# Optimization experiments

Hardware: AMD Instinct MI355X
Metric: run time of the kernel (lower is better)

## Reference

```python
import jax, jax.numpy as jnp
import numpy as np

LEAK = 0.95
THRESHOLD = 1.0
RESCALE = 2.0


def _xavier_uniform(key, shape, gain=2.0):
    fan_out, fan_in = shape
    bound = gain * np.sqrt(6.0 / (fan_in + fan_out))
    return jax.random.uniform(key, shape, jnp.float32, -bound, bound)


def setup_inputs() -> dict:
    key = jax.random.key(0)
    k_inp, k_w1, k_w2 = jax.random.split(key, 3)
    inp = jax.random.normal(k_inp, (8192, 784), jnp.float32)
    w1 = _xavier_uniform(k_w1, (800, 784))   # fc1.weight
    w2 = _xavier_uniform(k_w2, (10, 800))    # fc2.weight
    return {"inp": inp, "w1": w1, "w2": w2, "num_steps": 25}


@jax.custom_vjp
def spike_fn(x):
    return (x > 0).astype(x.dtype)

def _spike_fwd(x):
    return spike_fn(x), x

def _spike_bwd(x, g):
    # grad = g * 0.3 * relu(1 - |x|)  (surrogate BP)
    return (g * 0.3 * jnp.maximum(1.0 - jnp.abs(x), 0.0),)

spike_fn.defvjp(_spike_fwd, _spike_bwd)


def poisson_gen(key, inp):
    r = jax.random.uniform(key, inp.shape, inp.dtype)
    temp = (r * RESCALE <= jnp.abs(inp)).astype(inp.dtype) * jnp.sign(inp)
    return 0.5 * (temp + 1.0)


def reference(inp, w1, w2, num_steps):
    batch = inp.shape[0]
    x = inp.reshape(batch, -1)
    keys = jax.random.split(jax.random.key(42), num_steps)

    def step(carry, key):
        mem1, mem2 = carry
        sp = poisson_gen(key, x)                    # [B, 784]
        mem1 = LEAK * mem1 + (1.0 - LEAK) * (sp @ w1.T)  # [B, 800]
        mem_thr = mem1 / THRESHOLD - 1.0
        out = spike_fn(mem_thr)
        rst = jnp.where(mem_thr > 0, THRESHOLD, 0.0)
        mem1 = mem1 - jax.lax.stop_gradient(rst)
        mem2 = mem2 + out @ w2.T                    # [B, 10]
        return (mem1, mem2), None

    init = (jnp.zeros((batch, 800), x.dtype), jnp.zeros((batch, 10), x.dtype))
    (_, mem2), _ = jax.lax.scan(step, init, keys)
    return mem2 / num_steps
```

## Files before the change

### kernel.cpp

```cpp
#include <hip/hip_runtime.h>
#include <cstdint>

__host__ __device__ inline uint32_t tf_rotl32(uint32_t x, uint32_t r) {
  return (x << r) | (x >> (32u - r));
}

__host__ __device__ inline void threefry2x32(uint32_t k0, uint32_t k1,
                                             uint32_t x0, uint32_t x1,
                                             uint32_t* o0, uint32_t* o1) {
  uint32_t ks0 = k0, ks1 = k1, ks2 = k0 ^ k1 ^ 0x1BD11BDAu;
  x0 += ks0; x1 += ks1;
#define TF_R(r) { x0 += x1; x1 = tf_rotl32(x1, r); x1 ^= x0; }
  TF_R(13) TF_R(15) TF_R(26) TF_R(6)
  x0 += ks1; x1 += ks2 + 1u;
  TF_R(17) TF_R(29) TF_R(16) TF_R(24)
  x0 += ks2; x1 += ks0 + 2u;
  TF_R(13) TF_R(15) TF_R(26) TF_R(6)
  x0 += ks0; x1 += ks1 + 3u;
  TF_R(17) TF_R(29) TF_R(16) TF_R(24)
  x0 += ks1; x1 += ks2 + 4u;
  TF_R(13) TF_R(15) TF_R(26) TF_R(6)
  x0 += ks2; x1 += ks0 + 5u;
#undef TF_R
  *o0 = x0; *o1 = x1;
}

#define BSZ   8192
#define KIN   784
#define HID   800
#define NOUT  10
#define NSTEP 25


__global__ __launch_bounds__(256) void enc_kernel(const float* __restrict__ inp,
                                                  uint8_t* __restrict__ enc,
                                                  uint32_t k0, uint32_t k1) {
  int j = blockIdx.x * blockDim.x + threadIdx.x;
  if (j >= BSZ * KIN) return;
  uint32_t o0, o1;
  threefry2x32(k0, k1, 0u, (uint32_t)j, &o0, &o1);
  uint32_t bits = o0 ^ o1;
  float r = __uint_as_float((bits >> 9) | 0x3f800000u) - 1.0f;
  float x = inp[j];
  bool cond = (2.0f * r <= fabsf(x));
  int s = (x > 0.0f) ? 1 : ((x < 0.0f) ? -1 : 0);
  enc[j] = (uint8_t)(1 + (cond ? s : 0));
}

#define BM 128
#define BN 32
#define BK 8

typedef float f32x2 __attribute__((ext_vector_type(2)));

__device__ __forceinline__ float cvt_ub(uint32_t x, int i) {
  return (float)((x >> (8 * i)) & 0xffu);
}

__device__ __forceinline__ void pk_fma_lo(f32x2& acc, f32x2 a, f32x2 b) {
  asm("v_pk_fma_f32 %0, %1, %2, %0 op_sel:[0,0,0] op_sel_hi:[0,1,1]"
      : "+v"(acc)
      : "v"(a), "v"(b));
}
__device__ __forceinline__ void pk_fma_hi(f32x2& acc, f32x2 a, f32x2 b) {
  asm("v_pk_fma_f32 %0, %1, %2, %0 op_sel:[1,0,0] op_sel_hi:[1,1,1]"
      : "+v"(acc)
      : "v"(a), "v"(b));
}

__global__ __launch_bounds__(256) void gemm_kernel(const uint8_t* __restrict__ enc,
                                                   const float* __restrict__ w1,
                                                   float* __restrict__ gp) {
  __shared__ uint32_t As[2][BK][BM / 4];
  __shared__ float    Bs[2][BK][BN];
  const int panel  = blockIdx.z;
  const int kstart = (panel == 0) ? 0 : ((panel == 1) ? 264 : 528);
  const int ntile  = (panel == 2) ? 32 : 33;
  const int m0 = blockIdx.x * BM;
  const int n0 = blockIdx.y * BN;
  const int t  = threadIdx.x;

  const int tm = t / 8;
  const int tn = t % 8;

  const bool stA = (t < 64);
  const bool stB = (t >= 128 && t < 192);
  const int ar0 = (t & 31) * 4;
  const int ak0 = ((t >> 5) & 1) * 4;
  const int ub   = (t - 128) & 63;
  const int brow = ub & 31;
  const int bk0  = (ub >> 5) * 4;

  const uint8_t* aptr = enc + (size_t)(m0 + ar0) * KIN + kstart + ak0;
  const float*   bptr = w1 + (size_t)(n0 + brow) * KIN + kstart + bk0;

  uint32_t rA0, rA1, rA2, rA3;
  float4 rB;

  f32x2 acc[4][2];
#pragma unroll
  for (int mi = 0; mi < 4; mi++)
#pragma unroll
    for (int nj = 0; nj < 2; nj++) acc[mi][nj] = (f32x2)(0.0f);

#define LOAD_TILE(KOFF)                                              \
  {                                                                  \
    if (stA) {                                                       \
      const uint8_t* ap = aptr + (KOFF);                             \
      rA0 = *(const uint32_t*)(ap + (size_t)0 * KIN);                \
      rA1 = *(const uint32_t*)(ap + (size_t)1 * KIN);                \
      rA2 = *(const uint32_t*)(ap + (size_t)2 * KIN);                \
      rA3 = *(const uint32_t*)(ap + (size_t)3 * KIN);                \
    }                                                                \
    if (stB) rB = *(const float4*)(bptr + (KOFF));                   \
  }

#define STORE_TILE(P)                                                \
  {                                                                  \
    if (stA) {                                                       \
      uint32_t a01  = __builtin_amdgcn_perm(rA1, rA0, 0x05010400u);  \
      uint32_t a01h = __builtin_amdgcn_perm(rA1, rA0, 0x07030602u);  \
      uint32_t a23  = __builtin_amdgcn_perm(rA3, rA2, 0x05010400u);  \
      uint32_t a23h = __builtin_amdgcn_perm(rA3, rA2, 0x07030602u);  \
      As[P][ak0 + 0][ar0 >> 2] = __builtin_amdgcn_perm(a23,  a01,  0x05040100u); \
      As[P][ak0 + 1][ar0 >> 2] = __builtin_amdgcn_perm(a23,  a01,  0x07060302u); \
      As[P][ak0 + 2][ar0 >> 2] = __builtin_amdgcn_perm(a23h, a01h, 0x05040100u); \
      As[P][ak0 + 3][ar0 >> 2] = __builtin_amdgcn_perm(a23h, a01h, 0x07060302u); \
    }                                                                \
    if (stB) {                                                       \
      Bs[P][bk0 + 0][brow] = rB.x;                                   \
      Bs[P][bk0 + 1][brow] = rB.y;                                   \
      Bs[P][bk0 + 2][brow] = rB.z;                                   \
      Bs[P][bk0 + 3][brow] = rB.w;                                   \
    }                                                                \
  }

  LOAD_TILE(0)
  STORE_TILE(0)
  __syncthreads();

  int p = 0;
  for (int tile = 0; tile < ntile; tile++) {
    const bool more = (tile + 1 < ntile);
    if (more) { LOAD_TILE((size_t)(tile + 1) * BK) }
    {
      const uint32_t* arow = &As[p][0][tm];
      const float*    brw  = &Bs[p][0][tn * 4];
#pragma unroll
      for (int kk = 0; kk < BK; kk++) {
        uint32_t aw = arow[(size_t)kk * (BM / 4)];
        float4 bv = *(const float4*)(brw + (size_t)kk * BN);
        f32x2 am[2];
        am[0].x = cvt_ub(aw, 0); am[0].y = cvt_ub(aw, 1);
        am[1].x = cvt_ub(aw, 2); am[1].y = cvt_ub(aw, 3);
        f32x2 b2[2];
        b2[0].x = bv.x; b2[0].y = bv.y;
        b2[1].x = bv.z; b2[1].y = bv.w;
#pragma unroll
        for (int mp = 0; mp < 2; mp++) {
          pk_fma_lo(acc[2 * mp + 0][0], am[mp], b2[0]);
          pk_fma_lo(acc[2 * mp + 0][1], am[mp], b2[1]);
          pk_fma_hi(acc[2 * mp + 1][0], am[mp], b2[0]);
          pk_fma_hi(acc[2 * mp + 1][1], am[mp], b2[1]);
        }
      }
    }
    if (more) { STORE_TILE(p ^ 1) }
    __syncthreads();
    p ^= 1;
  }
#undef LOAD_TILE
#undef STORE_TILE

  float* base = gp + (size_t)panel * BSZ * HID;
#pragma unroll
  for (int mi = 0; mi < 4; mi++) {
    float* dst = base + (size_t)(m0 + tm * 4 + mi) * HID + n0 + tn * 4;
    float4 o;
    o.x = acc[mi][0].x;
    o.y = acc[mi][0].y;
    o.z = acc[mi][1].x;
    o.w = acc[mi][1].y;
    *(float4*)dst = o;
  }
}

__global__ __launch_bounds__(256) void update_kernel(const float* __restrict__ gp,
                                                     float* __restrict__ mem1,
                                                     const float* __restrict__ w2,
                                                     float* __restrict__ mem2) {
  __shared__ float w2s[NOUT * HID];
  for (int i = threadIdx.x; i < NOUT * HID; i += 256) w2s[i] = w2[i];
  __syncthreads();

  const int wave = threadIdx.x / 64;
  const int lane = threadIdx.x % 64;
  const int b = blockIdx.x * 4 + wave;

  const size_t GS = (size_t)BSZ * HID;
  const float* g0 = gp + (size_t)b * HID;
  const float* g1 = g0 + GS;
  const float* g2 = g1 + GS;
  float* mrow = mem1 + (size_t)b * HID;

  float acc[NOUT];
#pragma unroll
  for (int i = 0; i < NOUT; i++) acc[i] = 0.0f;

  for (int j = lane; j < HID; j += 64) {
    float gs = __fmul_rn(0.5f, __fadd_rn(__fadd_rn(g0[j], g1[j]), g2[j]));
    float m = __fadd_rn(__fmul_rn(0.95f, mrow[j]), __fmul_rn(0.05f, gs));
    bool spike = __fadd_rn(m, -1.0f) > 0.0f;
    mrow[j] = spike ? __fadd_rn(m, -1.0f) : m;
    if (spike) {
#pragma unroll
      for (int i = 0; i < NOUT; i++) acc[i] += w2s[i * HID + j];
    }
  }
#pragma unroll
  for (int i = 0; i < NOUT; i++) {
    float v = acc[i];
    for (int off = 32; off > 0; off >>= 1) v += __shfl_down(v, off);
    if (lane == 0) mem2[(size_t)b * NOUT + i] += v;
  }
}

__global__ __launch_bounds__(256) void finalize_kernel(const float* __restrict__ mem2,
                                                       const int* __restrict__ ns,
                                                       float* __restrict__ out) {
  int i = blockIdx.x * blockDim.x + threadIdx.x;
  if (i < BSZ * NOUT) out[i] = mem2[i] / (float)(*ns);
}

extern "C" void kernel_launch(void* const* d_in, const int* in_sizes, int n_in,
                              void* d_out, int out_size, void* d_ws, size_t ws_size,
                              hipStream_t stream) {
  const float* inp = (const float*)d_in[0];
  const float* w1  = (const float*)d_in[1];
  const float* w2  = (const float*)d_in[2];
  const int*   dns = (const int*)d_in[3];
  float* out = (float*)d_out;

  char* ws = (char*)d_ws;
  size_t off = 0;
  uint8_t* enc = (uint8_t*)(ws + off);  off += (size_t)BSZ * KIN;
  off = (off + 255) & ~(size_t)255;
  float* gp   = (float*)(ws + off);     off += (size_t)3 * BSZ * HID * 4;
  float* mem1 = (float*)(ws + off);     off += (size_t)BSZ * HID * 4;
  float* mem2 = (float*)(ws + off);     off += (size_t)BSZ * NOUT * 4;

  (void)hipMemsetAsync(mem1, 0, (size_t)BSZ * HID * 4, stream);
  (void)hipMemsetAsync(mem2, 0, (size_t)BSZ * NOUT * 4, stream);

  uint32_t keys[NSTEP][2];
  for (int t = 0; t < NSTEP; t++)
    threefry2x32(0u, 42u, 0u, (uint32_t)t, &keys[t][0], &keys[t][1]);

  const int n_elem = BSZ * KIN;
  for (int t = 0; t < NSTEP; t++) {
    enc_kernel<<<(n_elem + 255) / 256, 256, 0, stream>>>(inp, enc, keys[t][0], keys[t][1]);
    gemm_kernel<<<dim3(BSZ / BM, HID / BN, 3), 256, 0, stream>>>(enc, w1, gp);
    update_kernel<<<BSZ / 4, 256, 0, stream>>>(gp, mem1, w2, mem2);
  }
  finalize_kernel<<<(BSZ * NOUT + 255) / 256, 256, 0, stream>>>(mem2, dns, out);
}
```

Baseline: 4.681 ms.

## Load GEMM tiles directly into LDS with global_load_lds and row-major A layout

Replaces register-staged global loads plus byte permutes and LDS stores with direct global-to-LDS DMA loads issued by two wavefronts. The A tile is stored row-major so each thread reads its four rows with two 128-bit LDS loads and extracts bytes per k step. This is meant to remove register staging, permute instructions and explicit LDS writes. In exchange it relies on the barrier waiting for the asynchronous LDS writes, and it uses narrow 4-byte DMA transactions.

After: 4.857 ms. +3.8%, slower.

```diff
diff --git a/kernel.cpp b/kernel.cpp
--- a/kernel.cpp
+++ b/kernel.cpp
@@ -52,9 +52,16 @@
 #define BK 8
 
 typedef float f32x2 __attribute__((ext_vector_type(2)));
-
-__device__ __forceinline__ float cvt_ub(uint32_t x, int i) {
+typedef uint32_t u32;
+
+__device__ __forceinline__ float cvt_ub(u32 x, int i) {
   return (float)((x >> (8 * i)) & 0xffu);
+}
+
+__device__ __forceinline__ void gload4(const void* g, void* l) {
+  __builtin_amdgcn_global_load_lds(
+      (const __attribute__((address_space(1))) void*)g,
+      (__attribute__((address_space(3))) void*)l, 4, 0, 0);
 }
 
 __device__ __forceinline__ void pk_fma_lo(f32x2& acc, f32x2 a, f32x2 b) {
@@ -71,31 +78,22 @@
 __global__ __launch_bounds__(256) void gemm_kernel(const uint8_t* __restrict__ enc,
                                                    const float* __restrict__ w1,
                                                    float* __restrict__ gp) {
-  __shared__ uint32_t As[2][BK][BM / 4];
-  __shared__ float    Bs[2][BK][BN];
+  __shared__ u32   As[2][BK * BM / 4];
+  __shared__ float Bs[2][BK][BN];
   const int panel  = blockIdx.z;
-  const int kstart = (panel == 0) ? 0 : ((panel == 1) ? 264 : 528);
+  const int kstart = panel * 264;
   const int ntile  = (panel == 2) ? 32 : 33;
   const int m0 = blockIdx.x * BM;
   const int n0 = blockIdx.y * BN;
   const int t  = threadIdx.x;
+  const int lane = t & 63;
+  const int wv   = t >> 6;
 
   const int tm = t / 8;
   const int tn = t % 8;
 
-  const bool stA = (t < 64);
-  const bool stB = (t >= 128 && t < 192);
-  const int ar0 = (t & 31) * 4;
-  const int ak0 = ((t >> 5) & 1) * 4;
-  const int ub   = (t - 128) & 63;
-  const int brow = ub & 31;
-  const int bk0  = (ub >> 5) * 4;
-
-  const uint8_t* aptr = enc + (size_t)(m0 + ar0) * KIN + kstart + ak0;
-  const float*   bptr = w1 + (size_t)(n0 + brow) * KIN + kstart + bk0;
-
-  uint32_t rA0, rA1, rA2, rA3;
-  float4 rB;
+  const uint8_t* a_src = enc + (size_t)(m0 + (lane >> 1)) * KIN + kstart + (lane & 1) * 4;
+  const float*   b_src = w1  + (size_t)(n0 + (lane & 31)) * KIN + kstart + (lane >> 5);
 
   f32x2 acc[4][2];
 #pragma unroll
@@ -103,74 +101,55 @@
 #pragma unroll
     for (int nj = 0; nj < 2; nj++) acc[mi][nj] = (f32x2)(0.0f);
 
-#define LOAD_TILE(KOFF)                                              \
-  {                                                                  \
-    if (stA) {                                                       \
-      const uint8_t* ap = aptr + (KOFF);                             \
-      rA0 = *(const uint32_t*)(ap + (size_t)0 * KIN);                \
-      rA1 = *(const uint32_t*)(ap + (size_t)1 * KIN);                \
-      rA2 = *(const uint32_t*)(ap + (size_t)2 * KIN);                \
-      rA3 = *(const uint32_t*)(ap + (size_t)3 * KIN);                \
-    }                                                                \
-    if (stB) rB = *(const float4*)(bptr + (KOFF));                   \
-  }
-
-#define STORE_TILE(P)                                                \
-  {                                                                  \
-    if (stA) {                                                       \
-      uint32_t a01  = __builtin_amdgcn_perm(rA1, rA0, 0x05010400u);  \
-      uint32_t a01h = __builtin_amdgcn_perm(rA1, rA0, 0x07030602u);  \
-      uint32_t a23  = __builtin_amdgcn_perm(rA3, rA2, 0x05010400u);  \
-      uint32_t a23h = __builtin_amdgcn_perm(rA3, rA2, 0x07030602u);  \
-      As[P][ak0 + 0][ar0 >> 2] = __builtin_amdgcn_perm(a23,  a01,  0x05040100u); \
-      As[P][ak0 + 1][ar0 >> 2] = __builtin_amdgcn_perm(a23,  a01,  0x07060302u); \
-      As[P][ak0 + 2][ar0 >> 2] = __builtin_amdgcn_perm(a23h, a01h, 0x05040100u); \
-      As[P][ak0 + 3][ar0 >> 2] = __builtin_amdgcn_perm(a23h, a01h, 0x07060302u); \
-    }                                                                \
-    if (stB) {                                                       \
-      Bs[P][bk0 + 0][brow] = rB.x;                                   \
-      Bs[P][bk0 + 1][brow] = rB.y;                                   \
-      Bs[P][bk0 + 2][brow] = rB.z;                                   \
-      Bs[P][bk0 + 3][brow] = rB.w;                                   \
-    }                                                                \
-  }
-
-  LOAD_TILE(0)
-  STORE_TILE(0)
+#define ISSUE(P, TILE)                                                    \
+  {                                                                       \
+    if (wv == 0) {                                                        \
+      _Pragma("unroll")                                                   \
+      for (int q = 0; q < 4; q++)                                         \
+        gload4(a_src + (size_t)(TILE) * BK + (size_t)(32 * q) * KIN,      \
+               &As[P][64 * q]);                                           \
+    } else if (wv == 1) {                                                 \
+      _Pragma("unroll")                                                   \
+      for (int q = 0; q < 4; q++)                                         \
+        gload4(b_src + (size_t)(TILE) * BK + 2 * q, &Bs[P][2 * q][0]);    \
+    }                                                                     \
+  }
+
+  ISSUE(0, 0)
   __syncthreads();
 
   int p = 0;
   for (int tile = 0; tile < ntile; tile++) {
-    const bool more = (tile + 1 < ntile);
-    if (more) { LOAD_TILE((size_t)(tile + 1) * BK) }
-    {
-      const uint32_t* arow = &As[p][0][tm];
-      const float*    brw  = &Bs[p][0][tn * 4];
-#pragma unroll
-      for (int kk = 0; kk < BK; kk++) {
-        uint32_t aw = arow[(size_t)kk * (BM / 4)];
-        float4 bv = *(const float4*)(brw + (size_t)kk * BN);
-        f32x2 am[2];
-        am[0].x = cvt_ub(aw, 0); am[0].y = cvt_ub(aw, 1);
-        am[1].x = cvt_ub(aw, 2); am[1].y = cvt_ub(aw, 3);
-        f32x2 b2[2];
-        b2[0].x = bv.x; b2[0].y = bv.y;
-        b2[1].x = bv.z; b2[1].y = bv.w;
-#pragma unroll
-        for (int mp = 0; mp < 2; mp++) {
-          pk_fma_lo(acc[2 * mp + 0][0], am[mp], b2[0]);
-          pk_fma_lo(acc[2 * mp + 0][1], am[mp], b2[1]);
-          pk_fma_hi(acc[2 * mp + 1][0], am[mp], b2[0]);
-          pk_fma_hi(acc[2 * mp + 1][1], am[mp], b2[1]);
-        }
+    if (tile + 1 < ntile) { ISSUE(p ^ 1, tile + 1) }
+    const u32* aw = &As[p][tm * 8];
+    uint4 qa = *(const uint4*)(aw);
+    uint4 qb = *(const uint4*)(aw + 4);
+#pragma unroll
+    for (int kk = 0; kk < BK; kk++) {
+      const u32 w0  = (kk < 4) ? qa.x : qa.y;
+      const u32 w1r = (kk < 4) ? qa.z : qa.w;
+      const u32 w2  = (kk < 4) ? qb.x : qb.y;
+      const u32 w3  = (kk < 4) ? qb.z : qb.w;
+      const int sh = kk & 3;
+      f32x2 am[2];
+      am[0].x = cvt_ub(w0, sh);  am[0].y = cvt_ub(w1r, sh);
+      am[1].x = cvt_ub(w2, sh);  am[1].y = cvt_ub(w3, sh);
+      float4 bv = *(const float4*)&Bs[p][kk][tn * 4];
+      f32x2 b2[2];
+      b2[0].x = bv.x; b2[0].y = bv.y;
+      b2[1].x = bv.z; b2[1].y = bv.w;
+#pragma unroll
+      for (int mp = 0; mp < 2; mp++) {
+        pk_fma_lo(acc[2 * mp + 0][0], am[mp], b2[0]);
+        pk_fma_lo(acc[2 * mp + 0][1], am[mp], b2[1]);
+        pk_fma_hi(acc[2 * mp + 1][0], am[mp], b2[0]);
+        pk_fma_hi(acc[2 * mp + 1][1], am[mp], b2[1]);
       }
     }
-    if (more) { STORE_TILE(p ^ 1) }
     __syncthreads();
     p ^= 1;
   }
-#undef LOAD_TILE
-#undef STORE_TILE
+#undef ISSUE
 
   float* base = gp + (size_t)panel * BSZ * HID;
 #pragma unroll
```
